# Kernel optimization log

Hardware: AMD Instinct MI355X
Metric: run time of the kernel (lower is better)

The kernel has to match this reference:

```python
import jax, jax.numpy as jnp
import numpy as np
import math


def _selective_scan(u, delta, A, Bs, Cs, D, delta_bias):
    """Mamba selective scan.
    u, delta: (B,K,Dn,L); A: (K,Dn,N); Bs, Cs: (B,K,N,L); D, delta_bias: (K,Dn).
    delta_softplus=True semantics from selective_scan_fn.
    """
    delta = jax.nn.softplus(delta + delta_bias[None, :, :, None])
    dl = jnp.moveaxis(delta, -1, 0)  # (L,B,K,Dn)
    ul = jnp.moveaxis(u, -1, 0)      # (L,B,K,Dn)
    bl = jnp.moveaxis(Bs, -1, 0)     # (L,B,K,N)
    cl = jnp.moveaxis(Cs, -1, 0)     # (L,B,K,N)
    h0 = jnp.zeros(u.shape[:3] + (A.shape[-1],), u.dtype)  # (B,K,Dn,N)

    def step(h, inp):
        d, ut, bt, ct = inp
        h = jnp.exp(d[..., None] * A) * h + (d * ut)[..., None] * bt[:, :, None, :]
        y = jnp.einsum('bkdn,bkn->bkd', h, ct)
        return h, y

    _, ys = jax.lax.scan(step, h0, (dl, ul, bl, cl))
    return jnp.moveaxis(ys, 0, -1) + D[None, :, :, None] * u  # (B,K,Dn,L)


def setup_inputs() -> dict:
    key = jax.random.key(0)
    B, H, W, C = 8, 64, 64, 192
    Dn, N, R, K = 192, 8, 12, 4
    ks = jax.random.split(key, 8)
    x = jax.random.normal(ks[0], (B, H, W, C), jnp.float32)
    in_proj_w = jax.random.normal(ks[1], (2 * Dn, C), jnp.float32) * (C ** -0.5)
    conv_w = jax.random.normal(ks[2], (Dn, 1, 3, 3), jnp.float32) * 0.2
    conv_b = jnp.zeros((Dn,), jnp.float32)
    x_proj_w = jax.random.normal(ks[3], (K, R + 2 * N, Dn), jnp.float32) * (Dn ** -0.5)
    dt_std = R ** -0.5
    dt_projs_w = jax.random.uniform(ks[4], (K, Dn, R), jnp.float32, -dt_std, dt_std)
    dt = jnp.exp(jax.random.uniform(ks[5], (K, Dn), jnp.float32)
                 * (math.log(0.1) - math.log(0.001)) + math.log(0.001))
    dt = jnp.clip(dt, 1e-4, None)
    dt_projs_b = dt + jnp.log(-jnp.expm1(-dt))  # inverse softplus
    A_logs = jnp.broadcast_to(jnp.log(jnp.arange(1, N + 1, dtype=jnp.float32)), (K, Dn, N)).copy()
    Ds = jnp.ones((K, Dn), jnp.float32)
    ln_w = jnp.ones((Dn,), jnp.float32)
    ln_b = jnp.zeros((Dn,), jnp.float32)
    out_proj_w = jax.random.normal(ks[6], (C, Dn), jnp.float32) * (Dn ** -0.5)
    return {"x": x, "in_proj_w": in_proj_w, "conv_w": conv_w, "conv_b": conv_b,
            "x_proj_w": x_proj_w, "dt_projs_w": dt_projs_w, "dt_projs_b": dt_projs_b,
            "A_logs": A_logs, "Ds": Ds, "ln_w": ln_w, "ln_b": ln_b,
            "out_proj_w": out_proj_w}


def reference(x, in_proj_w, conv_w, conv_b, x_proj_w, dt_projs_w, dt_projs_b,
              A_logs, Ds, ln_w, ln_b, out_proj_w):
    B, H, W, C = x.shape
    K, _, Dn = x_proj_w.shape
    N = A_logs.shape[-1]
    R = dt_projs_w.shape[-1]
    L = H * W

    xz = x @ in_proj_w.T                       # (B,H,W,2*Dn)
    xf, z = jnp.split(xz, 2, axis=-1)
    xc = jnp.transpose(xf, (0, 3, 1, 2))       # (B,Dn,H,W)
    xc = jax.lax.conv_general_dilated(
        xc, conv_w, (1, 1), [(1, 1), (1, 1)],
        feature_group_count=Dn,
        dimension_numbers=('NCHW', 'OIHW', 'NCHW')) + conv_b[None, :, None, None]
    xc = jax.nn.silu(xc)

    # 4-directional scan sequences: hw, wh, reversed-hw, reversed-wh
    x_hw = xc.reshape(B, Dn, L)
    x_wh = jnp.transpose(xc, (0, 1, 3, 2)).reshape(B, Dn, L)
    x2 = jnp.stack([x_hw, x_wh], axis=1)
    xs = jnp.concatenate([x2, jnp.flip(x2, axis=-1)], axis=1)  # (B,4,Dn,L)

    x_dbl = jnp.einsum('bkdl,kcd->bkcl', xs, x_proj_w)
    dts, Bsx, Csx = jnp.split(x_dbl, [R, R + N], axis=2)
    dts = jnp.einsum('bkrl,kdr->bkdl', dts, dt_projs_w)

    A = -jnp.exp(A_logs)                       # (K,Dn,N)
    out_y = _selective_scan(xs, dts, A, Bsx, Csx, Ds, dt_projs_b)  # (B,4,Dn,L)

    inv_y = jnp.flip(out_y[:, 2:4], axis=-1)
    wh_y = jnp.transpose(out_y[:, 1].reshape(B, Dn, W, H), (0, 1, 3, 2)).reshape(B, Dn, L)
    invwh_y = jnp.transpose(inv_y[:, 1].reshape(B, Dn, W, H), (0, 1, 3, 2)).reshape(B, Dn, L)
    y = out_y[:, 0] + inv_y[:, 0] + wh_y + invwh_y  # (B,Dn,L)

    y = jnp.transpose(y, (0, 2, 1)).reshape(B, H, W, Dn)
    mu = y.mean(-1, keepdims=True)
    var = y.var(-1, keepdims=True)
    y = (y - mu) / jnp.sqrt(var + 1e-5) * ln_w + ln_b
    y = y * jax.nn.silu(z)
    return y @ out_proj_w.T
```

## Files before the change

kernel.cpp:

```cpp
#include <hip/hip_runtime.h>
#include <hip/hip_bf16.h>

constexpr int B_  = 8;
constexpr int H_  = 64;
constexpr int W_  = 64;
constexpr int C_  = 192;
constexpr int Dn  = 192;
constexpr int Nst = 8;
constexpr int R_  = 12;
constexpr int K_  = 4;
constexpr int L_  = H_ * W_;
constexpr int CS  = 32;
constexpr int GS  = 8;
constexpr int NC  = L_ / CS;
constexpr int CPROJ = R_ + 2 * Nst;
constexpr int MROWS = B_ * L_;

typedef __attribute__((ext_vector_type(8))) short short8v;
typedef __attribute__((ext_vector_type(4))) float f32x4;
typedef __attribute__((ext_vector_type(2))) float f32x2;

__device__ __forceinline__ int map_t(int k, int t) {
    int tt = (k >= 2) ? (L_ - 1 - t) : t;
    if (k & 1) tt = (tt & 63) * 64 + (tt >> 6);
    return tt;
}

__device__ __forceinline__ short f2bf(float f) {
    unsigned u = __float_as_uint(f);
    u += 0x7FFFu + ((u >> 16) & 1u);
    return (short)(u >> 16);
}
__device__ __forceinline__ float bf2f(short s) {
    return __uint_as_float(((unsigned)(unsigned short)s) << 16);
}

__device__ __forceinline__ f32x2 mk2(float a, float b) { f32x2 v; v.x = a; v.y = b; return v; }
__device__ __forceinline__ f32x2 lo2(float4 v) { return mk2(v.x, v.y); }
__device__ __forceinline__ f32x2 hi2(float4 v) { return mk2(v.z, v.w); }
__device__ __forceinline__ f32x2 pkfma(f32x2 a, f32x2 b, f32x2 c) {
    return __builtin_elementwise_fma(a, b, c);
}

constexpr int WOFF_IN  = 0;
constexpr int WOFF_XP  = 73728;
constexpr int WOFF_OUT = 95232;
constexpr int WTOTAL   = 132096;
constexpr int XUNITS   = MROWS * Dn / 8;
constexpr int WUNITS   = WTOTAL / 8;
__global__ __launch_bounds__(256) void k_cvt(const float* __restrict__ x,
                                             const float* __restrict__ w_in,
                                             const float* __restrict__ xpw,
                                             const float* __restrict__ wout,
                                             short* __restrict__ x_bf,
                                             short* __restrict__ w_bf) {
    int g = blockIdx.x * 256 + threadIdx.x;
    const float* src;
    short* dst;
    int off;
    if (g < XUNITS) { src = x; dst = x_bf; off = g * 8; }
    else {
        g -= XUNITS;
        if (g >= WUNITS) return;
        int base = g * 8;
        dst = w_bf; off = base;
        if (base < WOFF_XP)       { src = w_in; }
        else if (base < WOFF_OUT) { src = xpw;  src -= WOFF_XP; }
        else                      { src = wout; src -= WOFF_OUT; }
    }
    float4 a = *reinterpret_cast<const float4*>(src + off);
    float4 b = *reinterpret_cast<const float4*>(src + off + 4);
    short8v v = {f2bf(a.x), f2bf(a.y), f2bf(a.z), f2bf(a.w),
                 f2bf(b.x), f2bf(b.y), f2bf(b.z), f2bf(b.w)};
    *reinterpret_cast<short8v*>(dst + off) = v;
}

__device__ __forceinline__ void mgemm_core(const short* __restrict__ A,
                                           const short* __restrict__ Wb,
                                           f32x4 (&acc)[4][2],
                                           int mrow, int ncol, int Nact, int K) {
    const int lane = threadIdx.x & 63;
    const int koff = (lane >> 4) * 8;
    for (int k0 = 0; k0 < K; k0 += 32) {
        short8v af[4], bfr[2];
#pragma unroll
        for (int mf = 0; mf < 4; mf++)
            af[mf] = *reinterpret_cast<const short8v*>(
                A + (size_t)(mrow + mf * 16) * K + k0 + koff);
#pragma unroll
        for (int nf = 0; nf < 2; nf++) {
            int r = ncol + nf * 16;
            short8v z = {0, 0, 0, 0, 0, 0, 0, 0};
            bfr[nf] = (r < Nact)
                ? *reinterpret_cast<const short8v*>(Wb + (size_t)r * K + k0 + koff)
                : z;
        }
#pragma unroll
        for (int mf = 0; mf < 4; mf++)
#pragma unroll
            for (int nf = 0; nf < 2; nf++)
                acc[mf][nf] = __builtin_amdgcn_mfma_f32_16x16x32_bf16(
                    af[mf], bfr[nf], acc[mf][nf], 0, 0, 0);
    }
}

__global__ __launch_bounds__(256) void k_mgemm_f(const short* __restrict__ A,
                                                 const short* __restrict__ Wb,
                                                 float* __restrict__ out0,
                                                 int Nact, int K) {
    const int m0 = blockIdx.x * 128, n0 = blockIdx.y * 64;
    const int wid = threadIdx.x >> 6, lane = threadIdx.x & 63;
    const int wm = wid >> 1, wn = wid & 1;
    f32x4 acc[4][2] = {};
    mgemm_core(A, Wb, acc, m0 + wm * 64 + (lane & 15), n0 + wn * 32 + (lane & 15),
               Nact, K);
    const int prow = (lane >> 4) * 4, pcol = lane & 15;
#pragma unroll
    for (int mf = 0; mf < 4; mf++) {
        int mbase = m0 + wm * 64 + mf * 16 + prow;
#pragma unroll
        for (int nf = 0; nf < 2; nf++) {
            int n = n0 + wn * 32 + nf * 16 + pcol;
            if (n >= Nact) continue;
#pragma unroll
            for (int r = 0; r < 4; r++)
                out0[(size_t)(mbase + r) * Nact + n] = acc[mf][nf][r];
        }
    }
}

__global__ __launch_bounds__(256) void k_mgemm_in(const short* __restrict__ A,
                                                  const short* __restrict__ Wb,
                                                  short* __restrict__ xf_bf,
                                                  short* __restrict__ z_bf,
                                                  int K) {
    const int m0 = blockIdx.x * 128, n0 = blockIdx.y * 64;
    const int wid = threadIdx.x >> 6, lane = threadIdx.x & 63;
    const int wm = wid >> 1, wn = wid & 1;
    f32x4 acc[4][2] = {};
    mgemm_core(A, Wb, acc, m0 + wm * 64 + (lane & 15), n0 + wn * 32 + (lane & 15),
               384, K);
    const int prow = (lane >> 4) * 4, pcol = lane & 15;
#pragma unroll
    for (int mf = 0; mf < 4; mf++) {
        int mbase = m0 + wm * 64 + mf * 16 + prow;
#pragma unroll
        for (int nf = 0; nf < 2; nf++) {
            int n = n0 + wn * 32 + nf * 16 + pcol;
#pragma unroll
            for (int r = 0; r < 4; r++) {
                int m = mbase + r;
                if (n < 192) xf_bf[(size_t)m * 192 + n] = f2bf(acc[mf][nf][r]);
                else         z_bf[(size_t)m * 192 + (n - 192)] = f2bf(acc[mf][nf][r]);
            }
        }
    }
}

__global__ __launch_bounds__(256) void k_conv(const short* __restrict__ xfb,
                                              const float* __restrict__ cw,
                                              const float* __restrict__ cb,
                                              short* __restrict__ xcb) {
    size_t i = (size_t)blockIdx.x * 256 + threadIdx.x;
    int d = (int)(i % Dn);
    int p = (int)(i / Dn);
    int w = p & 63; p >>= 6;
    int h = p & 63; p >>= 6;
    int b = p;
    float acc = cb[d];
#pragma unroll
    for (int kh = 0; kh < 3; kh++) {
        int hh = h + kh - 1;
        if (hh < 0 || hh >= H_) continue;
#pragma unroll
        for (int kw = 0; kw < 3; kw++) {
            int ww = w + kw - 1;
            if (ww < 0 || ww >= W_) continue;
            acc = fmaf(bf2f(xfb[(((size_t)b * H_ + hh) * W_ + ww) * Dn + d]),
                       cw[d * 9 + kh * 3 + kw], acc);
        }
    }
    float sig = 1.f / (1.f + __expf(-acc));
    xcb[i] = f2bf(acc * sig);
}

__device__ __forceinline__ void delta_e1(float x, float& delta, float& e1) {
    float t = __expf(fminf(x, 80.f));
    float opt = 1.f + t;
    delta = __logf(opt);
    e1 = __builtin_amdgcn_rcpf(opt);
}

__device__ __forceinline__ float dot12p(const float4& q0, const float4& q1,
                                        const float4& q2, const f32x2* w2,
                                        float bias) {
    f32x2 a0 = pkfma(lo2(q0), w2[0], mk2(bias, 0.f));
    f32x2 a1 = lo2(q1) * w2[2];
    a0 = pkfma(hi2(q0), w2[1], a0);
    a1 = pkfma(hi2(q1), w2[3], a1);
    a0 = pkfma(lo2(q2), w2[4], a0);
    a1 = pkfma(hi2(q2), w2[5], a1);
    f32x2 s = a0 + a1;
    return s.x + s.y;
}

__device__ __forceinline__ float dot12(const float4& a, const float4& b,
                                       const float4& c, const float* w, float x) {
    x = fmaf(a.x, w[0], x);  x = fmaf(a.y, w[1], x);
    x = fmaf(a.z, w[2], x);  x = fmaf(a.w, w[3], x);
    x = fmaf(b.x, w[4], x);  x = fmaf(b.y, w[5], x);
    x = fmaf(b.z, w[6], x);  x = fmaf(b.w, w[7], x);
    x = fmaf(c.x, w[8], x);  x = fmaf(c.y, w[9], x);
    x = fmaf(c.z, w[10], x); x = fmaf(c.w, w[11], x);
    return x;
}

__global__ __launch_bounds__(192, 4) void k_scan1(const short* __restrict__ xcb,
                                               const float* __restrict__ xdbl,
                                               const float* __restrict__ dtw_all,
                                               const float* __restrict__ dtb_all,
                                               const float* __restrict__ alog,
                                               float* __restrict__ Aprod,
                                               float* __restrict__ hpart) {
    const int blk = blockIdx.x;
    const int c = blk % NC;
    const int k = (blk / NC) % K_;
    const int b = blk / (NC * K_);
    const int d = threadIdx.x;
    const int t0 = c * CS;
    const int stride = ((k & 1) ? 64 : 1) * ((k >= 2) ? -1 : 1);
    const int lm0 = map_t(k, t0);

    __shared__ float4 sx4[CS][5];
    const float4* xd4 = reinterpret_cast<const float4*>(xdbl);
    for (int i = d; i < CS * 5; i += 192) {
        int ts = i / 5, q = i % 5;
        sx4[ts][q] = xd4[((size_t)b * L_ + lm0 + ts * stride) * 28 + k * 7 + q];
    }
    __syncthreads();

    float dtw[R_];
#pragma unroll
    for (int r = 0; r < R_; r++) dtw[r] = dtw_all[((size_t)k * Dn + d) * R_ + r];
    f32x2 w2[6];
#pragma unroll
    for (int r = 0; r < 6; r++) w2[r] = mk2(dtw[2 * r], dtw[2 * r + 1]);
    const float bias = dtb_all[k * Dn + d];
    float Av[Nst];
    bool fast = true;
#pragma unroll
    for (int n = 0; n < Nst; n++) {
        Av[n] = -__expf(alog[((size_t)k * Dn + d) * Nst + n]);
        fast = fast && (fabsf(Av[n] + (float)(n + 1)) < 1e-3f);
    }

    const long stepD = (long)stride * Dn;
    const short* up = xcb + ((size_t)b * L_ + lm0) * Dn + d;
    size_t base = ((((size_t)(b * K_ + k) * NC + c) * Dn + d)) * Nst;

    if (fast) {
        f32x2 h01 = mk2(0.f, 0.f), h23 = h01, h45 = h01, h67 = h01;
        float p0 = 1.f, p1 = 1.f, p2_ = 1.f, p3_ = 1.f;
        for (int g = 0; g < CS / GS; ++g) {
            const short* ug = up + (long)g * GS * stepD;
            float e1a[GS], dua[GS];
#pragma unroll
            for (int j = 0; j < GS; ++j) {
                int ts = g * GS + j;
                float u = bf2f(ug[(long)j * stepD]);
                float4 q0 = sx4[ts][0], q1 = sx4[ts][1], q2 = sx4[ts][2];
                float delta, e1; delta_e1(dot12p(q0, q1, q2, w2, bias), delta, e1);
                e1a[j] = e1;
                dua[j] = delta * u;
            }
#pragma unroll
            for (int j = 0; j < GS; ++j) {
                int ts = g * GS + j;
                float e1 = e1a[j], du = dua[j];
                float4 qb0 = sx4[ts][3], qb1 = sx4[ts][4];
                float a2 = e1 * e1;
                f32x2 p12 = mk2(e1, a2);
                f32x2 a22 = mk2(a2, a2);
                f32x2 p34 = a22 * p12;
                f32x2 a44 = mk2(p34.y, p34.y);
                f32x2 p56 = a44 * p12;
                f32x2 p78 = a44 * p34;
                f32x2 du2 = mk2(du, du);
                h01 = pkfma(p12, h01, du2 * lo2(qb0));
                h23 = pkfma(p34, h23, du2 * hi2(qb0));
                h45 = pkfma(p56, h45, du2 * lo2(qb1));
                h67 = pkfma(p78, h67, du2 * hi2(qb1));
            }
            p0 *= e1a[0]; p1 *= e1a[1]; p2_ *= e1a[2]; p3_ *= e1a[3];
            p0 *= e1a[4]; p1 *= e1a[5]; p2_ *= e1a[6]; p3_ *= e1a[7];
        }
        float e1p = (p0 * p1) * (p2_ * p3_);
        float p2 = e1p * e1p, p3 = p2 * e1p, p4 = p2 * p2;
        float4* ap4 = reinterpret_cast<float4*>(Aprod + base);
        ap4[0] = make_float4(e1p, p2, p3, p4);
        ap4[1] = make_float4(p4 * e1p, p4 * p2, p4 * p3, p4 * p4);
        float4* hp4 = reinterpret_cast<float4*>(hpart + base);
        hp4[0] = make_float4(h01.x, h01.y, h23.x, h23.y);
        hp4[1] = make_float4(h45.x, h45.y, h67.x, h67.y);
    } else {
        float h[Nst] = {};
        float Ap[Nst];
#pragma unroll
        for (int n = 0; n < Nst; n++) Ap[n] = 1.f;
        float u_next = bf2f(*up);
        const short* upp = up;
        for (int ts = 0; ts < CS; ts++) {
            float u = u_next;
            upp += stepD;
            if (ts + 1 < CS) u_next = bf2f(*upp);
            float4 q0 = sx4[ts][0], q1 = sx4[ts][1], q2 = sx4[ts][2];
            float4 qb0 = sx4[ts][3], qb1 = sx4[ts][4];
            float Bv[Nst] = {qb0.x, qb0.y, qb0.z, qb0.w, qb1.x, qb1.y, qb1.z, qb1.w};
            float delta, e1; delta_e1(dot12(q0, q1, q2, dtw, bias), delta, e1);
            float du = delta * u;
#pragma unroll
            for (int n = 0; n < Nst; n++) {
                float a = __expf(delta * Av[n]);
                Ap[n] *= a;
                h[n] = fmaf(a, h[n], du * Bv[n]);
            }
        }
#pragma unroll
        for (int n = 0; n < Nst; n++) { Aprod[base + n] = Ap[n]; hpart[base + n] = h[n]; }
    }
}

__global__ __launch_bounds__(256) void k_scan2(const float* __restrict__ Aprod,
                                               const float* __restrict__ hpart,
                                               float* __restrict__ hin) {
    int idx = blockIdx.x * 256 + threadIdx.x;
    int dn = idx % (Dn * Nst);
    int bk = idx / (Dn * Nst);
    size_t stride = (size_t)Dn * Nst;
    size_t base = (size_t)bk * NC * stride + dn;
    float h = 0.f;
    for (int cc = 0; cc < NC; cc++) {
        size_t s = base + (size_t)cc * stride;
        hin[s] = h;
        h = fmaf(Aprod[s], h, hpart[s]);
    }
}

__global__ __launch_bounds__(192, 4) void k_scan3(const short* __restrict__ xcb,
                                               const float* __restrict__ xdbl,
                                               const float* __restrict__ dtw_all,
                                               const float* __restrict__ dtb_all,
                                               const float* __restrict__ alog,
                                               const float* __restrict__ dvec,
                                               const float* __restrict__ hin,
                                               short* __restrict__ y0,
                                               short* __restrict__ y1,
                                               short* __restrict__ y2,
                                               short* __restrict__ y3) {
    const int blk = blockIdx.x;
    const int c = blk % NC;
    const int k = (blk / NC) % K_;
    const int b = blk / (NC * K_);
    const int d = threadIdx.x;
    const int t0 = c * CS;
    const int stride = ((k & 1) ? 64 : 1) * ((k >= 2) ? -1 : 1);
    const int lm0 = map_t(k, t0);
    short* __restrict__ yk = (k == 0) ? y0 : (k == 1) ? y1 : (k == 2) ? y2 : y3;

    __shared__ float4 sx4[CS][7];
    const float4* xd4 = reinterpret_cast<const float4*>(xdbl);
    for (int i = d; i < CS * 7; i += 192) {
        int ts = i / 7, q = i % 7;
        sx4[ts][q] = xd4[((size_t)b * L_ + lm0 + ts * stride) * 28 + k * 7 + q];
    }
    __syncthreads();

    float dtw[R_];
#pragma unroll
    for (int r = 0; r < R_; r++) dtw[r] = dtw_all[((size_t)k * Dn + d) * R_ + r];
    f32x2 w2[6];
#pragma unroll
    for (int r = 0; r < 6; r++) w2[r] = mk2(dtw[2 * r], dtw[2 * r + 1]);
    const float bias = dtb_all[k * Dn + d];
    const float Dk = dvec[k * Dn + d];
    float Av[Nst];
    bool fast = true;
#pragma unroll
    for (int n = 0; n < Nst; n++) {
        Av[n] = -__expf(alog[((size_t)k * Dn + d) * Nst + n]);
        fast = fast && (fabsf(Av[n] + (float)(n + 1)) < 1e-3f);
    }

    size_t hbase = ((((size_t)(b * K_ + k) * NC + c) * Dn + d)) * Nst;
    const long stepD = (long)stride * Dn;
    const short* up = xcb + ((size_t)b * L_ + lm0) * Dn + d;
    short* yp = yk + ((size_t)b * L_ + lm0) * Dn + d;

    if (fast) {
        const float4* hi4 = reinterpret_cast<const float4*>(hin + hbase);
        float4 ha = hi4[0], hb = hi4[1];
        f32x2 h01 = lo2(ha), h23 = hi2(ha), h45 = lo2(hb), h67 = hi2(hb);
        for (int g = 0; g < CS / GS; ++g) {
            const short* ug = up + (long)g * GS * stepD;
            short* yg = yp + (long)g * GS * stepD;
            float e1a[GS], dua[GS], dku[GS];
#pragma unroll
            for (int j = 0; j < GS; ++j) {
                int ts = g * GS + j;
                float u = bf2f(ug[(long)j * stepD]);
                float4 q0 = sx4[ts][0], q1 = sx4[ts][1], q2 = sx4[ts][2];
                float delta, e1; delta_e1(dot12p(q0, q1, q2, w2, bias), delta, e1);
                e1a[j] = e1;
                dua[j] = delta * u;
                dku[j] = Dk * u;
            }
#pragma unroll
            for (int j = 0; j < GS; ++j) {
                int ts = g * GS + j;
                float e1 = e1a[j], du = dua[j];
                float4 qb0 = sx4[ts][3], qb1 = sx4[ts][4];
                float4 qc0 = sx4[ts][5], qc1 = sx4[ts][6];
                float a2 = e1 * e1;
                f32x2 p12 = mk2(e1, a2);
                f32x2 a22 = mk2(a2, a2);
                f32x2 p34 = a22 * p12;
                f32x2 a44 = mk2(p34.y, p34.y);
                f32x2 p56 = a44 * p12;
                f32x2 p78 = a44 * p34;
                f32x2 du2 = mk2(du, du);
                h01 = pkfma(p12, h01, du2 * lo2(qb0));
                h23 = pkfma(p34, h23, du2 * hi2(qb0));
                h45 = pkfma(p56, h45, du2 * lo2(qb1));
                h67 = pkfma(p78, h67, du2 * hi2(qb1));
                f32x2 yacc = mk2(dku[j], 0.f);
                yacc = pkfma(h01, lo2(qc0), yacc);
                yacc = pkfma(h23, hi2(qc0), yacc);
                yacc = pkfma(h45, lo2(qc1), yacc);
                yacc = pkfma(h67, hi2(qc1), yacc);
                yg[(long)j * stepD] = f2bf(yacc.x + yacc.y);
            }
        }
    } else {
        float h[Nst];
#pragma unroll
        for (int n = 0; n < Nst; n++) h[n] = hin[hbase + n];
        float u_next = bf2f(*up);
        const short* upp = up;
        short* ypp = yp;
        for (int ts = 0; ts < CS; ts++) {
            float u = u_next;
            upp += stepD;
            if (ts + 1 < CS) u_next = bf2f(*upp);
            float4 q0 = sx4[ts][0], q1 = sx4[ts][1], q2 = sx4[ts][2];
            float4 qb0 = sx4[ts][3], qb1 = sx4[ts][4];
            float4 qc0 = sx4[ts][5], qc1 = sx4[ts][6];
            float Bv[Nst] = {qb0.x, qb0.y, qb0.z, qb0.w, qb1.x, qb1.y, qb1.z, qb1.w};
            float Cv[Nst] = {qc0.x, qc0.y, qc0.z, qc0.w, qc1.x, qc1.y, qc1.z, qc1.w};
            float delta, e1; delta_e1(dot12(q0, q1, q2, dtw, bias), delta, e1);
            float du = delta * u;
            float y = Dk * u;
#pragma unroll
            for (int n = 0; n < Nst; n++) {
                float a = __expf(delta * Av[n]);
                h[n] = fmaf(a, h[n], du * Bv[n]);
                y = fmaf(h[n], Cv[n], y);
            }
            *ypp = f2bf(y);
            ypp += stepD;
        }
    }
}

__global__ __launch_bounds__(256) void k_ln(const short* __restrict__ y0,
                                            const short* __restrict__ y1,
                                            const short* __restrict__ y2,
                                            const short* __restrict__ y3,
                                            const short* __restrict__ zb,
                                            const float* __restrict__ lnw,
                                            const float* __restrict__ lnb,
                                            short* __restrict__ yfin) {
    const int row = blockIdx.x * 4 + (threadIdx.x >> 6);
    const int lane = threadIdx.x & 63;
    const size_t base = (size_t)row * Dn;
    float v[3];
    float s = 0.f, s2 = 0.f;
#pragma unroll
    for (int j = 0; j < 3; j++) {
        size_t idx = base + lane + j * 64;
        v[j] = bf2f(y0[idx]) + bf2f(y1[idx]) + bf2f(y2[idx]) + bf2f(y3[idx]);
        s += v[j];
        s2 = fmaf(v[j], v[j], s2);
    }
#pragma unroll
    for (int o = 1; o < 64; o <<= 1) {
        s += __shfl_xor(s, o);
        s2 += __shfl_xor(s2, o);
    }
    const float inv = 1.f / 192.f;
    float mu = s * inv;
    float var = s2 * inv - mu * mu;
    float rstd = rsqrtf(var + 1e-5f);
#pragma unroll
    for (int j = 0; j < 3; j++) {
        int dd = lane + j * 64;
        size_t idx = base + dd;
        float zz = bf2f(zb[idx]);
        float sig = 1.f / (1.f + __expf(-zz));
        float res = ((v[j] - mu) * rstd * lnw[dd] + lnb[dd]) * (zz * sig);
        yfin[idx] = f2bf(res);
    }
}

extern "C" void kernel_launch(void* const* d_in, const int* in_sizes, int n_in,
                              void* d_out, int out_size, void* d_ws, size_t ws_size,
                              hipStream_t stream) {
    const float* x    = (const float*)d_in[0];
    const float* w_in = (const float*)d_in[1];
    const float* cw   = (const float*)d_in[2];
    const float* cb   = (const float*)d_in[3];
    const float* xpw  = (const float*)d_in[4];
    const float* dtw  = (const float*)d_in[5];
    const float* dtb  = (const float*)d_in[6];
    const float* alog = (const float*)d_in[7];
    const float* dvec = (const float*)d_in[8];
    const float* lnw  = (const float*)d_in[9];
    const float* lnb  = (const float*)d_in[10];
    const float* wout = (const float*)d_in[11];
    float* out = (float*)d_out;

    const size_t SH  = (size_t)MROWS * Dn;
    const size_t SCN = (size_t)B_ * K_ * NC * Dn * Nst;

    char* p = (char*)d_ws;
    short* x_bf  = (short*)p; p += SH * 2;
    short* xf_bf = (short*)p; p += SH * 2;
    short* z_bf  = (short*)p; p += SH * 2;
    short* xc_bf = (short*)p; p += SH * 2;
    float* xdbl  = (float*)p; p += (size_t)MROWS * (K_ * CPROJ) * 4;
    float* Aprod = (float*)p; p += SCN * 4;
    float* hpart = (float*)p; p += SCN * 4;
    float* hin   = (float*)p; p += SCN * 4;
    short* w_bf  = (short*)p;
    short* y0 = x_bf;
    short* y1 = xf_bf;
    short* y2 = (short*)Aprod;
    short* y3 = (short*)hpart;
    short* yfin_bf = (short*)hin;

    k_cvt<<<(XUNITS + WUNITS + 255) / 256, 256, 0, stream>>>(x, w_in, xpw, wout,
                                                             x_bf, w_bf);
    k_mgemm_in<<<dim3(MROWS / 128, 6), 256, 0, stream>>>(x_bf, w_bf + WOFF_IN,
                                                         xf_bf, z_bf, C_);
    k_conv<<<(int)(SH / 256), 256, 0, stream>>>(xf_bf, cw, cb, xc_bf);
    k_mgemm_f<<<dim3(MROWS / 128, 2), 256, 0, stream>>>(xc_bf, w_bf + WOFF_XP,
                                                        xdbl, K_ * CPROJ, Dn);
    k_scan1<<<B_ * K_ * NC, 192, 0, stream>>>(xc_bf, xdbl, dtw, dtb, alog, Aprod, hpart);
    k_scan2<<<(B_ * K_ * Dn * Nst) / 256, 256, 0, stream>>>(Aprod, hpart, hin);
    k_scan3<<<B_ * K_ * NC, 192, 0, stream>>>(xc_bf, xdbl, dtw, dtb, alog, dvec,
                                              hin, y0, y1, y2, y3);
    k_ln<<<MROWS / 4, 256, 0, stream>>>(y0, y1, y2, y3, z_bf, lnw, lnb, yfin_bf);
    k_mgemm_f<<<dim3(MROWS / 128, 3), 256, 0, stream>>>(yfin_bf, w_bf + WOFF_OUT,
                                                        out, C_, Dn);
}
```

Measured before the change: 239.5 us.

## Tile depthwise conv over 8-row strips with vectorized 4-channel loads

Rewrites the depthwise 3x3 conv kernel so each thread handles 4 channels with short4 loads and computes 8 consecutive output rows along H. It keeps a 3x10 register window of inputs, so each input is reused across rows instead of reloaded 9 times per output. Weights and bias are loaded once per thread. The cost is higher register pressure and a much smaller grid (1024 blocks of 192 threads), which may lower occupancy.

```diff
diff --git a/kernel.cpp b/kernel.cpp
--- a/kernel.cpp
+++ b/kernel.cpp
@@ -157,31 +157,70 @@
     }
 }
 
-__global__ __launch_bounds__(256) void k_conv(const short* __restrict__ xfb,
+__global__ __launch_bounds__(192) void k_conv(const short* __restrict__ xfb,
                                               const float* __restrict__ cw,
                                               const float* __restrict__ cb,
                                               short* __restrict__ xcb) {
-    size_t i = (size_t)blockIdx.x * 256 + threadIdx.x;
-    int d = (int)(i % Dn);
-    int p = (int)(i / Dn);
-    int w = p & 63; p >>= 6;
-    int h = p & 63; p >>= 6;
-    int b = p;
-    float acc = cb[d];
-#pragma unroll
-    for (int kh = 0; kh < 3; kh++) {
-        int hh = h + kh - 1;
-        if (hh < 0 || hh >= H_) continue;
-#pragma unroll
-        for (int kw = 0; kw < 3; kw++) {
-            int ww = w + kw - 1;
-            if (ww < 0 || ww >= W_) continue;
-            acc = fmaf(bf2f(xfb[(((size_t)b * H_ + hh) * W_ + ww) * Dn + d]),
-                       cw[d * 9 + kh * 3 + kw], acc);
-        }
-    }
-    float sig = 1.f / (1.f + __expf(-acc));
-    xcb[i] = f2bf(acc * sig);
+    const int tid = threadIdx.x;
+    const int dg = tid % 48;
+    const int wl = tid / 48;
+    const int blk = blockIdx.x;
+    const int wq = blk & 15;
+    const int hq = (blk >> 4) & 7;
+    const int b  = blk >> 7;
+    const int w  = wq * 4 + wl;
+    const int d  = dg * 4;
+    const int h0 = hq * 8;
+
+    short4 win[3][10];
+    const short4 z4 = make_short4(0, 0, 0, 0);
+#pragma unroll
+    for (int kw = 0; kw < 3; kw++) {
+        int ww = w + kw - 1;
+        bool wok = (unsigned)ww < (unsigned)W_;
+        int wc = min(max(ww, 0), W_ - 1);
+#pragma unroll
+        for (int r = 0; r < 10; r++) {
+            int hh = h0 - 1 + r;
+            bool ok = wok && ((unsigned)hh < (unsigned)H_);
+            int hc = min(max(hh, 0), H_ - 1);
+            short4 v = *reinterpret_cast<const short4*>(
+                xfb + (((size_t)b * H_ + hc) * W_ + wc) * Dn + d);
+            win[kw][r] = ok ? v : z4;
+        }
+    }
+
+    float wgt[4][9];
+    float bias[4];
+#pragma unroll
+    for (int c = 0; c < 4; c++) {
+        bias[c] = cb[d + c];
+#pragma unroll
+        for (int t = 0; t < 9; t++) wgt[c][t] = cw[(d + c) * 9 + t];
+    }
+
+#pragma unroll
+    for (int j = 0; j < 8; j++) {
+        float a0 = bias[0], a1 = bias[1], a2 = bias[2], a3 = bias[3];
+#pragma unroll
+        for (int kh = 0; kh < 3; kh++)
+#pragma unroll
+            for (int kw = 0; kw < 3; kw++) {
+                short4 v = win[kw][j + kh];
+                int t = kh * 3 + kw;
+                a0 = fmaf(bf2f(v.x), wgt[0][t], a0);
+                a1 = fmaf(bf2f(v.y), wgt[1][t], a1);
+                a2 = fmaf(bf2f(v.z), wgt[2][t], a2);
+                a3 = fmaf(bf2f(v.w), wgt[3][t], a3);
+            }
+        short4 o;
+        o.x = f2bf(a0 / (1.f + __expf(-a0)));
+        o.y = f2bf(a1 / (1.f + __expf(-a1)));
+        o.z = f2bf(a2 / (1.f + __expf(-a2)));
+        o.w = f2bf(a3 / (1.f + __expf(-a3)));
+        *reinterpret_cast<short4*>(
+            xcb + (((size_t)b * H_ + h0 + j) * W_ + w) * Dn + d) = o;
+    }
 }
 
 __device__ __forceinline__ void delta_e1(float x, float& delta, float& e1) {
@@ -551,7 +590,7 @@
                                                              x_bf, w_bf);
     k_mgemm_in<<<dim3(MROWS / 128, 6), 256, 0, stream>>>(x_bf, w_bf + WOFF_IN,
                                                          xf_bf, z_bf, C_);
-    k_conv<<<(int)(SH / 256), 256, 0, stream>>>(xf_bf, cw, cb, xc_bf);
+    k_conv<<<B_ * (H_ / 8) * (W_ / 4), 192, 0, stream>>>(xf_bf, cw, cb, xc_bf);
     k_mgemm_f<<<dim3(MROWS / 128, 2), 256, 0, stream>>>(xc_bf, w_bf + WOFF_XP,
                                                         xdbl, K_ * CPROJ, Dn);
     k_scan1<<<B_ * K_ * NC, 192, 0, stream>>>(xc_bf, xdbl, dtw, dtb, alog, Aprod, hpart);
```

Result: faster. 201.6 us (median of 2 runs) (-15.8%).
